# Performance work log

Measured on AMD Instinct MI355X. Metric: run time of the kernel, lower is better.

The kernel has to match this reference:

```python
import jax, jax.numpy as jnp
import numpy as np

D_MODEL = 1024
N_HEADS = 16
D_HEAD = D_MODEL // N_HEADS


def setup_inputs() -> dict:
    key = jax.random.key(0)
    ks = jax.random.split(key, 11)
    B, L = 2, 2048
    s = 1.0 / np.sqrt(D_MODEL)
    return {
        "query": jax.random.normal(ks[0], (B, L, D_MODEL), jnp.float32),
        "key": jax.random.normal(ks[1], (B, L, D_MODEL), jnp.float32),
        "value": jax.random.normal(ks[2], (B, L, D_MODEL), jnp.float32),
        "Wq": jax.random.normal(ks[3], (D_MODEL, D_MODEL), jnp.float32) * s,
        "bq": jnp.zeros((D_MODEL,), jnp.float32),
        "Wk": jax.random.normal(ks[4], (D_MODEL, D_MODEL), jnp.float32) * s,
        "bk": jnp.zeros((D_MODEL,), jnp.float32),
        "Wv": jax.random.normal(ks[5], (D_MODEL, D_MODEL), jnp.float32) * s,
        "bv": jnp.zeros((D_MODEL,), jnp.float32),
        "Wo": jax.random.normal(ks[6], (D_MODEL, D_MODEL), jnp.float32) * s,
        "bo": jnp.zeros((D_MODEL,), jnp.float32),
    }


def reference(query, key, value, Wq, bq, Wk, bk, Wv, bv, Wo, bo):
    B, Lq, _ = query.shape
    Lk = key.shape[1]
    scale = D_HEAD ** -0.5
    # projections; weights stored as [in, out] (torch Linear applies x @ W.T; here W is already transposed)
    q = (query @ Wq + bq).reshape(B, Lq, N_HEADS, D_HEAD).transpose(0, 2, 1, 3)  # [B,H,Lq,dh]
    k = (key @ Wk + bk).reshape(B, Lk, N_HEADS, D_HEAD).transpose(0, 2, 1, 3)
    v = (value @ Wv + bv).reshape(B, Lk, N_HEADS, D_HEAD).transpose(0, 2, 1, 3)
    scores = jnp.einsum('bhqd,bhkd->bhqk', q, k) * scale  # [B,H,Lq,Lk]
    # causal mask (is_causal=True)
    causal = jnp.triu(jnp.ones((Lq, Lk), dtype=bool), k=1)
    scores = jnp.where(causal, -jnp.inf, scores)
    attn = jax.nn.softmax(scores, axis=-1)
    out = jnp.einsum('bhqk,bhkd->bhqd', attn, v)  # [B,H,Lq,dh]
    out = out.transpose(0, 2, 1, 3).reshape(B, Lq, D_MODEL)
    return out @ Wo + bo
```

## Files before the change

### kernel.cpp

```cpp
#include <hip/hip_runtime.h>
#include <hip/hip_bf16.h>

typedef __bf16 bf16x8 __attribute__((ext_vector_type(8)));
typedef __bf16 bf16x4 __attribute__((ext_vector_type(4)));
typedef float floatx4 __attribute__((ext_vector_type(4)));

#define MFMA16(a, b, c) __builtin_amdgcn_mfma_f32_16x16x32_bf16(a, b, c, 0, 0, 0)
#define AS1 __attribute__((address_space(1)))
#define AS3 __attribute__((address_space(3)))

constexpr int D = 1024;
constexpr int L = 2048;
constexpr int BB = 2;
constexpr int DH = 64;
constexpr float NEG_BIG = -1e30f;
constexpr float SCALE_LOG2E = 0.125f * 1.4426950408889634f;

__device__ __forceinline__ void gld16(const __bf16* g, __bf16* l) {
  __builtin_amdgcn_global_load_lds((AS1 void*)g, (AS3 void*)l, 16, 0, 0);
}

__global__ __launch_bounds__(256) void cvt_x(const float* __restrict__ xq, const float* __restrict__ xk,
                                             const float* __restrict__ xv, __bf16* __restrict__ out) {
  const int z = blockIdx.z;
  const float* src = z == 0 ? xq : z == 1 ? xk : xv;
  __bf16* dst = out + (size_t)z * BB * L * D;
  const int N = BB * L * D;
  const int stride = gridDim.x * 256 * 4;
  for (int i = (blockIdx.x * 256 + threadIdx.x) * 4; i < N; i += stride) {
    float4 f = *(const float4*)&src[i];
    bf16x4 b = {(__bf16)f.x, (__bf16)f.y, (__bf16)f.z, (__bf16)f.w};
    *(bf16x4*)&dst[i] = b;
  }
}

__global__ void transpose_w(const float* __restrict__ w0, const float* __restrict__ w1,
                            const float* __restrict__ w2, const float* __restrict__ w3,
                            __bf16* __restrict__ out) {
  __shared__ __bf16 tile[32][33];
  int mat = blockIdx.z;
  const float* src = mat == 0 ? w0 : mat == 1 ? w1 : mat == 2 ? w2 : w3;
  __bf16* dst = out + (size_t)mat * D * D;
  int bx = blockIdx.x * 32, by = blockIdx.y * 32;
  int tx = threadIdx.x, ty = threadIdx.y;
#pragma unroll
  for (int i = 0; i < 32; i += 8)
    tile[ty + i][tx] = (__bf16)src[(size_t)(by + ty + i) * D + bx + tx];
  __syncthreads();
#pragma unroll
  for (int i = 0; i < 32; i += 8)
    dst[(size_t)(bx + ty + i) * D + by + tx] = tile[tx][ty + i];
}

__device__ __forceinline__ void stage32(const __bf16* __restrict__ A, const __bf16* __restrict__ Bt,
                                        __bf16* sA, __bf16* sB, int m0, int n0, int kb,
                                        int r, int sc, int dst) {
  gld16(&A[(size_t)(m0 + r) * 1024 + kb + sc],       &sA[dst]);
  gld16(&A[(size_t)(m0 + 64 + r) * 1024 + kb + sc],  &sA[2048 + dst]);
  gld16(&Bt[(size_t)(n0 + r) * 1024 + kb + sc],      &sB[dst]);
  gld16(&Bt[(size_t)(n0 + 64 + r) * 1024 + kb + sc], &sB[2048 + dst]);
}

__device__ __forceinline__ void gemm_core(const __bf16* __restrict__ A, const __bf16* __restrict__ Bt,
                                          __bf16* sm, int m0, int n0, int wm, int wn,
                                          int l15, int quad, int t, floatx4 (&acc)[4][4]) {
  const int r = t >> 2;
  const int sc = ((t & 3) ^ ((r >> 1) & 3)) * 8;
  const int dst = t * 8;
  const int sw2 = (l15 >> 1) & 3;

  stage32(A, Bt, sm, sm + 8192, m0, n0, 0, r, sc, dst);

  int cur = 0;
  for (int kb = 0; kb < 1024; kb += 32) {
    if (kb + 32 < 1024) {
      stage32(A, Bt, sm + (cur ^ 1) * 4096, sm + 8192 + (cur ^ 1) * 4096, m0, n0, kb + 32, r, sc, dst);
      asm volatile("s_waitcnt vmcnt(4)" ::: "memory");
    } else {
      asm volatile("s_waitcnt vmcnt(0)" ::: "memory");
    }
    __builtin_amdgcn_s_barrier();

    const __bf16* sAc = sm + cur * 4096;
    const __bf16* sBc = sm + 8192 + cur * 4096;
    bf16x8 af[4], bf_[4];
#pragma unroll
    for (int i = 0; i < 4; i++) {
      const int row = wm * 64 + i * 16 + l15;
      af[i] = *(const bf16x8*)&sAc[(row * 4 + (quad ^ sw2)) * 8];
    }
#pragma unroll
    for (int j = 0; j < 4; j++) {
      const int row = wn * 64 + j * 16 + l15;
      bf_[j] = *(const bf16x8*)&sBc[(row * 4 + (quad ^ sw2)) * 8];
    }
    asm volatile("s_waitcnt lgkmcnt(0)" ::: "memory");
    __builtin_amdgcn_sched_barrier(0);
    __builtin_amdgcn_s_barrier();

#pragma unroll
    for (int i = 0; i < 4; i++)
#pragma unroll
      for (int j = 0; j < 4; j++)
        acc[i][j] = MFMA16(af[i], bf_[j], acc[i][j]);

    cur ^= 1;
  }
}

__global__ __launch_bounds__(256, 3) void gemm_proj(const __bf16* __restrict__ xc, const __bf16* __restrict__ wt,
                                                    const float* __restrict__ bq, const float* __restrict__ bk,
                                                    const float* __restrict__ bv, __bf16* __restrict__ qkv) {
  __shared__ __align__(16) __bf16 smem[17408];

  const int flat = (blockIdx.z * 32 + blockIdx.y) * 8 + blockIdx.x;
  const int s = (flat & 7) * 96 + (flat >> 3);
  const int z = s >> 8;
  const int rem = s & 255;
  const int by = rem >> 3, bx = rem & 7;

  const __bf16* A = xc + (size_t)z * BB * L * D;
  const __bf16* Bt = wt + (size_t)z * D * D;
  const float* bias = z == 0 ? bq : z == 1 ? bk : bv;
  __bf16* dst = qkv + (size_t)z * BB * L * D;

  const int t = threadIdx.x;
  const int lane = t & 63;
  const int w = t >> 6;
  const int wm = w >> 1, wn = w & 1;
  const int l15 = lane & 15, quad = lane >> 4;
  const int m0 = by * 128, n0 = bx * 128;

  floatx4 acc[4][4];
#pragma unroll
  for (int i = 0; i < 4; i++)
#pragma unroll
    for (int j = 0; j < 4; j++) acc[i][j] = (floatx4){0.f, 0.f, 0.f, 0.f};

  gemm_core(A, Bt, smem, m0, n0, wm, wn, l15, quad, t, acc);

  float bvv[4];
#pragma unroll
  for (int j = 0; j < 4; j++) bvv[j] = bias[n0 + wn * 64 + j * 16 + l15];

  constexpr int TP = 136;
  __bf16* T = smem;
  if (z < 2) {
#pragma unroll
    for (int i = 0; i < 4; i++) {
      const int mrowb = wm * 64 + i * 16 + quad * 4;
#pragma unroll
      for (int j = 0; j < 4; j++) {
        const int ccol = wn * 64 + j * 16 + l15;
#pragma unroll
        for (int rr = 0; rr < 4; rr++) {
          float val = acc[i][j][rr] + bvv[j];
          if (z == 0) val *= SCALE_LOG2E;
          T[(mrowb + rr) * TP + ccol] = (__bf16)val;
        }
      }
    }
  } else {
#pragma unroll
    for (int i = 0; i < 4; i++) {
      const int mrowb = wm * 64 + i * 16 + quad * 4;
#pragma unroll
      for (int j = 0; j < 4; j++) {
        const int ccol = wn * 64 + j * 16 + l15;
        bf16x4 v4;
#pragma unroll
        for (int rr = 0; rr < 4; rr++) v4[rr] = (__bf16)(acc[i][j][rr] + bvv[j]);
        *(bf16x4*)&T[ccol * TP + mrowb] = v4;
      }
    }
  }
  __syncthreads();

  const int b = m0 >> 11;
  const int l0 = m0 & 2047;
  if (z < 2) {
#pragma unroll
    for (int sH = 0; sH < 8; sH++) {
      const int c = sH * 256 + t;
      const int mrow = c >> 4, k16 = c & 15;
      const int h = (n0 >> 6) + (k16 >> 3);
      const int d0 = (k16 & 7) * 8;
      bf16x8 v = *(const bf16x8*)&T[mrow * TP + k16 * 8];
      *(bf16x8*)&dst[((size_t)(b * 16 + h) * 2048 + l0 + mrow) * 64 + d0] = v;
    }
  } else {
    const int R0 = (b * 16 + (n0 >> 6)) * 64;
#pragma unroll
    for (int sH = 0; sH < 8; sH++) {
      const int c = sH * 256 + t;
      const int ccol = c >> 4, k16 = c & 15;
      bf16x8 v = *(const bf16x8*)&T[ccol * TP + k16 * 8];
      *(bf16x8*)&dst[(size_t)(R0 + ccol) * 2048 + l0 + k16 * 8] = v;
    }
  }
}

__global__ __launch_bounds__(256, 3) void gemm_o(const __bf16* __restrict__ ctx, const __bf16* __restrict__ wto,
                                                 const float* __restrict__ bo, float* __restrict__ out) {
  __shared__ __align__(16) __bf16 smem[16384];

  const int flat = blockIdx.y * 8 + blockIdx.x;
  const int s = (flat & 7) * 32 + (flat >> 3);
  const int by = s >> 3, bx = s & 7;

  const int t = threadIdx.x;
  const int lane = t & 63;
  const int w = t >> 6;
  const int wm = w >> 1, wn = w & 1;
  const int l15 = lane & 15, quad = lane >> 4;
  const int m0 = by * 128, n0 = bx * 128;

  floatx4 acc[4][4];
#pragma unroll
  for (int i = 0; i < 4; i++)
#pragma unroll
    for (int j = 0; j < 4; j++) acc[i][j] = (floatx4){0.f, 0.f, 0.f, 0.f};

  gemm_core(ctx, wto, smem, m0, n0, wm, wn, l15, quad, t, acc);

  float bvv[4];
#pragma unroll
  for (int j = 0; j < 4; j++) bvv[j] = bo[n0 + wn * 64 + j * 16 + l15];

#pragma unroll
  for (int i = 0; i < 4; i++) {
    const int rowb = m0 + wm * 64 + i * 16 + quad * 4;
#pragma unroll
    for (int j = 0; j < 4; j++) {
      const int col = n0 + wn * 64 + j * 16 + l15;
#pragma unroll
      for (int rr = 0; rr < 4; rr++)
        out[(size_t)(rowb + rr) * 1024 + col] = acc[i][j][rr] + bvv[j];
    }
  }
}

__global__ __launch_bounds__(256, 2) void flash_attn(const __bf16* __restrict__ q, const __bf16* __restrict__ k,
                                                     const __bf16* __restrict__ vT, __bf16* __restrict__ ctx) {
  __shared__ __align__(16) __bf16 kbuf[2][4096];
  __shared__ __align__(16) __bf16 vbuf[2][4096];

  const int t = threadIdx.x;
  const int lane = t & 63;
  const int w = t >> 6;
  const int l15 = lane & 15, quad = lane >> 4;
  const int bh = blockIdx.y;
  const int p = (blockIdx.x + blockIdx.y) & 15;
  const int qtA = 31 - p;
  const int qtB = p;

  const __bf16* qb = q + (size_t)bh * L * DH;
  const __bf16* kb_ = k + (size_t)bh * L * DH;
  const __bf16* vb = vT + (size_t)bh * DH * L;

  const int c0 = t, c1 = 256 + t;
  const int kr0 = c0 >> 3, kd0 = ((c0 & 7) ^ (kr0 & 7)) * 8;
  const int kr1 = c1 >> 3, kd1 = ((c1 & 7) ^ (kr1 & 7)) * 8;

  const int qrA = qtA * 64 + w * 16 + l15;
  const int qrB = qtB * 64 + w * 16 + l15;
  const bf16x8 aqA0 = *(const bf16x8*)&qb[(size_t)qrA * 64 + quad * 8];
  const bf16x8 aqA1 = *(const bf16x8*)&qb[(size_t)qrA * 64 + 32 + quad * 8];
  const bf16x8 aqB0 = *(const bf16x8*)&qb[(size_t)qrB * 64 + quad * 8];
  const bf16x8 aqB1 = *(const bf16x8*)&qb[(size_t)qrB * 64 + 32 + quad * 8];

  floatx4 oA[4], oB[4];
#pragma unroll
  for (int nt = 0; nt < 4; nt++) {
    oA[nt] = (floatx4){0.f, 0.f, 0.f, 0.f};
    oB[nt] = (floatx4){0.f, 0.f, 0.f, 0.f};
  }
  float psA = 0.f, psB = 0.f;

  gld16(&kb_[(size_t)kr0 * 64 + kd0], &kbuf[0][c0 * 8]);
  gld16(&kb_[(size_t)kr1 * 64 + kd1], &kbuf[0][c1 * 8]);
  gld16(&vb[(size_t)kr0 * L + kd0],   &vbuf[0][c0 * 8]);
  gld16(&vb[(size_t)kr1 * L + kd1],   &vbuf[0][c1 * 8]);

#pragma unroll 1
  for (int it = 0; it <= qtA; ++it) {
    const int cur = it & 1;
    const int kt = it * 64;

    if (it < qtA) {
      const int ktn = kt + 64;
      gld16(&kb_[(size_t)(ktn + kr0) * 64 + kd0], &kbuf[cur ^ 1][c0 * 8]);
      gld16(&kb_[(size_t)(ktn + kr1) * 64 + kd1], &kbuf[cur ^ 1][c1 * 8]);
      gld16(&vb[(size_t)kr0 * L + ktn + kd0],     &vbuf[cur ^ 1][c0 * 8]);
      gld16(&vb[(size_t)kr1 * L + ktn + kd1],     &vbuf[cur ^ 1][c1 * 8]);
      asm volatile("s_waitcnt vmcnt(4)" ::: "memory");
    } else {
      asm volatile("s_waitcnt vmcnt(0)" ::: "memory");
    }
    __builtin_amdgcn_s_barrier();

    const bool diagA = (it == qtA);
    const bool doB   = (it <= qtB);
    const bool diagB = (it == qtB);

#pragma unroll
    for (int sp = 0; sp < 2; ++sp) {
      bf16x8 kf0[2], kf1[2];
#pragma unroll
      for (int u = 0; u < 2; ++u) {
        const int kr = (2 * sp + u) * 16 + l15;
        kf0[u] = *(const bf16x8*)&kbuf[cur][(kr * 8 + (quad ^ (kr & 7))) * 8];
        kf1[u] = *(const bf16x8*)&kbuf[cur][(kr * 8 + ((quad + 4) ^ (kr & 7))) * 8];
      }

      bf16x8 paA;
#pragma unroll
      for (int u = 0; u < 2; ++u) {
        floatx4 zz = (floatx4){0.f, 0.f, 0.f, 0.f};
        zz = MFMA16(kf0[u], aqA0, zz);
        zz = MFMA16(kf1[u], aqA1, zz);
        if (diagA) {
          const int kgb = kt + (2 * sp + u) * 16 + quad * 4;
#pragma unroll
          for (int rr = 0; rr < 4; rr++)
            if (kgb + rr > qrA) zz[rr] = NEG_BIG;
        }
#pragma unroll
        for (int rr = 0; rr < 4; rr++) {
          const float pv = __builtin_amdgcn_exp2f(zz[rr]);
          psA += pv;
          paA[u * 4 + rr] = (__bf16)pv;
        }
      }

      bf16x8 paB;
      if (doB) {
#pragma unroll
        for (int u = 0; u < 2; ++u) {
          floatx4 zz = (floatx4){0.f, 0.f, 0.f, 0.f};
          zz = MFMA16(kf0[u], aqB0, zz);
          zz = MFMA16(kf1[u], aqB1, zz);
          if (diagB) {
            const int kgb = kt + (2 * sp + u) * 16 + quad * 4;
#pragma unroll
            for (int rr = 0; rr < 4; rr++)
              if (kgb + rr > qrB) zz[rr] = NEG_BIG;
          }
#pragma unroll
          for (int rr = 0; rr < 4; rr++) {
            const float pv = __builtin_amdgcn_exp2f(zz[rr]);
            psB += pv;
            paB[u * 4 + rr] = (__bf16)pv;
          }
        }
      }

#pragma unroll
      for (int nt = 0; nt < 4; nt++) {
        const int d = nt * 16 + l15;
        const int x0 = (sp * 4 + (quad >> 1)) ^ (d & 7);
        const int x1 = (sp * 4 + 2 + (quad >> 1)) ^ (d & 7);
        union { bf16x8 v8; bf16x4 v4[2]; } uv;
        uv.v4[0] = *(const bf16x4*)&vbuf[cur][(d * 8 + x0) * 8 + (quad & 1) * 4];
        uv.v4[1] = *(const bf16x4*)&vbuf[cur][(d * 8 + x1) * 8 + (quad & 1) * 4];
        oA[nt] = MFMA16(paA, uv.v8, oA[nt]);
        if (doB) oB[nt] = MFMA16(paB, uv.v8, oB[nt]);
      }
    }

    asm volatile("s_waitcnt lgkmcnt(0)" ::: "memory");
    __builtin_amdgcn_sched_barrier(0);
    __builtin_amdgcn_s_barrier();
  }

  const int b = bh >> 4, h = bh & 15;

  psA += __shfl_xor(psA, 16);
  psA += __shfl_xor(psA, 32);
  const float invA = 1.f / psA;
#pragma unroll
  for (int rr = 0; rr < 4; rr++) {
    const float inv = __shfl(invA, (lane & 48) + quad * 4 + rr);
    const int row = qtA * 64 + w * 16 + quad * 4 + rr;
#pragma unroll
    for (int nt = 0; nt < 4; nt++) {
      const int col = h * 64 + nt * 16 + l15;
      ctx[((size_t)b * L + row) * 1024 + col] = (__bf16)(oA[nt][rr] * inv);
    }
  }

  psB += __shfl_xor(psB, 16);
  psB += __shfl_xor(psB, 32);
  const float invB = 1.f / psB;
#pragma unroll
  for (int rr = 0; rr < 4; rr++) {
    const float inv = __shfl(invB, (lane & 48) + quad * 4 + rr);
    const int row = qtB * 64 + w * 16 + quad * 4 + rr;
#pragma unroll
    for (int nt = 0; nt < 4; nt++) {
      const int col = h * 64 + nt * 16 + l15;
      ctx[((size_t)b * L + row) * 1024 + col] = (__bf16)(oB[nt][rr] * inv);
    }
  }
}

extern "C" void kernel_launch(void* const* d_in, const int* in_sizes, int n_in,
                              void* d_out, int out_size, void* d_ws, size_t ws_size,
                              hipStream_t stream) {
  const float* x_q = (const float*)d_in[0];
  const float* x_k = (const float*)d_in[1];
  const float* x_v = (const float*)d_in[2];
  const float* Wq  = (const float*)d_in[3];
  const float* bq  = (const float*)d_in[4];
  const float* Wk  = (const float*)d_in[5];
  const float* bk  = (const float*)d_in[6];
  const float* Wv  = (const float*)d_in[7];
  const float* bv  = (const float*)d_in[8];
  const float* Wo  = (const float*)d_in[9];
  const float* bo  = (const float*)d_in[10];

  char* ws = (char*)d_ws;
  __bf16* xc  = (__bf16*)ws;
  __bf16* wt  = (__bf16*)(ws + ((size_t)24 << 20));
  __bf16* qkv = (__bf16*)(ws + ((size_t)32 << 20));
  __bf16* ctx = (__bf16*)ws;
  __bf16* qp  = qkv;
  __bf16* kp  = qkv + (size_t)BB * L * D;
  __bf16* vtp = qkv + (size_t)2 * BB * L * D;

  cvt_x<<<dim3(1024, 1, 3), 256, 0, stream>>>(x_q, x_k, x_v, xc);
  transpose_w<<<dim3(32, 32, 4), dim3(32, 8), 0, stream>>>(Wq, Wk, Wv, Wo, wt);
  gemm_proj<<<dim3(8, 32, 3), 256, 0, stream>>>(xc, wt, bq, bk, bv, qkv);
  flash_attn<<<dim3(16, 32), 256, 0, stream>>>(qp, kp, vtp, ctx);
  gemm_o<<<dim3(8, 32), 256, 0, stream>>>(ctx, wt + (size_t)3 * D * D, bo, (float*)d_out);
}
```

Measured before the change: 213.5 us.

## Process two KV tiles per barrier with double-buffered 128-key stages

Restructures the flash attention main loop so each iteration stages and computes two 64-key K/V tiles, halving the number of barrier/wait points per query tile. LDS buffers grow to two halves per double buffer (64 KB total), and prefetch of the next pair of tiles overlaps with computing the current pair. This reduces synchronization overhead but the larger shared memory footprint may limit occupancy to fewer blocks per CU.

```diff
diff --git a/kernel.cpp b/kernel.cpp
--- a/kernel.cpp
+++ b/kernel.cpp
@@ -242,8 +242,8 @@
 
 __global__ __launch_bounds__(256, 2) void flash_attn(const __bf16* __restrict__ q, const __bf16* __restrict__ k,
                                                      const __bf16* __restrict__ vT, __bf16* __restrict__ ctx) {
-  __shared__ __align__(16) __bf16 kbuf[2][4096];
-  __shared__ __align__(16) __bf16 vbuf[2][4096];
+  __shared__ __align__(16) __bf16 kbuf[2][2][4096];
+  __shared__ __align__(16) __bf16 vbuf[2][2][4096];
 
   const int t = threadIdx.x;
   const int lane = t & 63;
@@ -277,31 +277,21 @@
   }
   float psA = 0.f, psB = 0.f;
 
-  gld16(&kb_[(size_t)kr0 * 64 + kd0], &kbuf[0][c0 * 8]);
-  gld16(&kb_[(size_t)kr1 * 64 + kd1], &kbuf[0][c1 * 8]);
-  gld16(&vb[(size_t)kr0 * L + kd0],   &vbuf[0][c0 * 8]);
-  gld16(&vb[(size_t)kr1 * L + kd1],   &vbuf[0][c1 * 8]);
-
-#pragma unroll 1
-  for (int it = 0; it <= qtA; ++it) {
-    const int cur = it & 1;
-    const int kt = it * 64;
-
-    if (it < qtA) {
-      const int ktn = kt + 64;
-      gld16(&kb_[(size_t)(ktn + kr0) * 64 + kd0], &kbuf[cur ^ 1][c0 * 8]);
-      gld16(&kb_[(size_t)(ktn + kr1) * 64 + kd1], &kbuf[cur ^ 1][c1 * 8]);
-      gld16(&vb[(size_t)kr0 * L + ktn + kd0],     &vbuf[cur ^ 1][c0 * 8]);
-      gld16(&vb[(size_t)kr1 * L + ktn + kd1],     &vbuf[cur ^ 1][c1 * 8]);
-      asm volatile("s_waitcnt vmcnt(4)" ::: "memory");
-    } else {
-      asm volatile("s_waitcnt vmcnt(0)" ::: "memory");
-    }
-    __builtin_amdgcn_s_barrier();
-
-    const bool diagA = (it == qtA);
-    const bool doB   = (it <= qtB);
-    const bool diagB = (it == qtB);
+  auto STAGE = [&](int buf, int half, int ktile) {
+    const int kt = ktile * 64;
+    gld16(&kb_[(size_t)(kt + kr0) * 64 + kd0], &kbuf[buf][half][c0 * 8]);
+    gld16(&kb_[(size_t)(kt + kr1) * 64 + kd1], &kbuf[buf][half][c1 * 8]);
+    gld16(&vb[(size_t)kr0 * L + kt + kd0],     &vbuf[buf][half][c0 * 8]);
+    gld16(&vb[(size_t)kr1 * L + kt + kd1],     &vbuf[buf][half][c1 * 8]);
+  };
+
+  auto COMPUTE = [&](int buf, int half, int ktile) {
+    const int kt = ktile * 64;
+    const bool diagA = (ktile == qtA);
+    const bool doB   = (ktile <= qtB);
+    const bool diagB = (ktile == qtB);
+    const __bf16* kbh = kbuf[buf][half];
+    const __bf16* vbh = vbuf[buf][half];
 
 #pragma unroll
     for (int sp = 0; sp < 2; ++sp) {
@@ -309,8 +299,8 @@
 #pragma unroll
       for (int u = 0; u < 2; ++u) {
         const int kr = (2 * sp + u) * 16 + l15;
-        kf0[u] = *(const bf16x8*)&kbuf[cur][(kr * 8 + (quad ^ (kr & 7))) * 8];
-        kf1[u] = *(const bf16x8*)&kbuf[cur][(kr * 8 + ((quad + 4) ^ (kr & 7))) * 8];
+        kf0[u] = *(const bf16x8*)&kbh[(kr * 8 + (quad ^ (kr & 7))) * 8];
+        kf1[u] = *(const bf16x8*)&kbh[(kr * 8 + ((quad + 4) ^ (kr & 7))) * 8];
       }
 
       bf16x8 paA;
@@ -361,12 +351,38 @@
         const int x0 = (sp * 4 + (quad >> 1)) ^ (d & 7);
         const int x1 = (sp * 4 + 2 + (quad >> 1)) ^ (d & 7);
         union { bf16x8 v8; bf16x4 v4[2]; } uv;
-        uv.v4[0] = *(const bf16x4*)&vbuf[cur][(d * 8 + x0) * 8 + (quad & 1) * 4];
-        uv.v4[1] = *(const bf16x4*)&vbuf[cur][(d * 8 + x1) * 8 + (quad & 1) * 4];
+        uv.v4[0] = *(const bf16x4*)&vbh[(d * 8 + x0) * 8 + (quad & 1) * 4];
+        uv.v4[1] = *(const bf16x4*)&vbh[(d * 8 + x1) * 8 + (quad & 1) * 4];
         oA[nt] = MFMA16(paA, uv.v8, oA[nt]);
         if (doB) oB[nt] = MFMA16(paB, uv.v8, oB[nt]);
       }
     }
+  };
+
+  const int ntiles = qtA + 1;
+  STAGE(0, 0, 0);
+  STAGE(0, 1, 1);
+
+  int it2 = 0;
+#pragma unroll 1
+  for (int base = 0; base < ntiles; base += 2, ++it2) {
+    const int cur = it2 & 1;
+    const int remn = ntiles - base - 2;
+
+    if (remn >= 2) {
+      STAGE(cur ^ 1, 0, base + 2);
+      STAGE(cur ^ 1, 1, base + 3);
+      asm volatile("s_waitcnt vmcnt(8)" ::: "memory");
+    } else if (remn == 1) {
+      STAGE(cur ^ 1, 0, base + 2);
+      asm volatile("s_waitcnt vmcnt(4)" ::: "memory");
+    } else {
+      asm volatile("s_waitcnt vmcnt(0)" ::: "memory");
+    }
+    __builtin_amdgcn_s_barrier();
+
+    COMPUTE(cur, 0, base);
+    if (base + 1 < ntiles) COMPUTE(cur, 1, base + 1);
 
     asm volatile("s_waitcnt lgkmcnt(0)" ::: "memory");
     __builtin_amdgcn_sched_barrier(0);
```

Result: faster. 206.2 us (-3.5%).
